# Optimization experiments

Hardware: AMD Instinct MI355X
Metric: run time of the kernel (lower is better)

## Reference

```python
import jax, jax.numpy as jnp
import numpy as np

B, C, L = 256, 512, 150
CI = C // 4            # channel_in = in_dim // 4 = 128
K = 150                # one_hot_cls_num (depthwise kernel over length)
POOL = 150             # MaxPool2d kernel (150, 1)
EPS = 1e-5             # BatchNorm eps


def setup_inputs() -> dict:
    key = jax.random.key(0)
    ks = jax.random.split(key, 8)
    n = lambda k, shape, s: jax.random.normal(k, shape, jnp.float32) * s
    return {
        "x":    jax.random.normal(ks[0], (B, C, L, 1), jnp.float32),
        "Wv":   n(ks[1], (CI, C), 0.06),   "bv": jnp.zeros((CI,), jnp.float32),
        "Wq":   n(ks[2], (CI, CI), 0.12),  "bq": jnp.zeros((CI,), jnp.float32),
        "Wk":   n(ks[3], (CI, CI), 0.12),  "bk": jnp.zeros((CI,), jnp.float32),
        "gamma": n(ks[4], (), 1.0),
        "Wd":   n(ks[5], (2 * CI, K), 0.1), "bd": jnp.zeros((2 * CI,), jnp.float32),
        "Wp":   n(ks[6], (2 * CI, 2 * CI), 0.08), "bp": jnp.zeros((2 * CI,), jnp.float32),
        "bn_g": jnp.ones((2 * CI,), jnp.float32),
        "bn_b": jnp.zeros((2 * CI,), jnp.float32),
    }


def reference(x, Wv, bv, Wq, bq, Wk, bk, gamma, Wd, bd, Wp, bp, bn_g, bn_b):
    xb = x[..., 0]                                             # [B, C, L] (trailing width==1)
    # 1x1 convs are per-position matmuls over the channel dim
    v = jnp.einsum('oc,bcl->bol', Wv, xb) + bv[:, None]        # [B, CI, L]
    q = jnp.einsum('oc,bcl->bol', Wq, v) + bq[:, None]         # [B, CI, L]
    k = jnp.einsum('oc,bcl->bol', Wk, v) + bk[:, None]         # [B, CI, L]
    # raw (unscaled) attention: energy = q^T k, softmax over keys
    energy = jnp.einsum('bci,bcj->bij', q, k)                  # [B, L, L]
    attn = jax.nn.softmax(energy, axis=-1)
    # x = bmm(v, attn^T): out[b,c,i] = sum_j v[b,c,j] * attn[b,i,j]
    att_out = jnp.einsum('bcj,bij->bci', v, attn)              # [B, CI, L]
    cat = jnp.concatenate([gamma * att_out, v], axis=1)        # [B, 2CI, L]
    # MaxPool2d kernel=(150,1), stride=(150,1) over length
    Lp = L // POOL
    y = cat[:, :, : Lp * POOL].reshape(B, 2 * CI, Lp, POOL).max(axis=-1)
    y = y.reshape(B, -1)                                       # [B, 2CI*Lp]
    # depthwise conv kernel (K,1), VALID padding, groups = 2CI
    dw = jax.lax.conv_general_dilated(
        cat[:, :, :, None],                                    # [B, 2CI, L, 1]
        Wd[:, None, :, None],                                  # [2CI, 1, K, 1]
        window_strides=(1, 1), padding='VALID',
        dimension_numbers=('NCHW', 'OIHW', 'NCHW'),
        feature_group_count=2 * CI,
    ) + bd[None, :, None, None]                                # [B, 2CI, L-K+1, 1]
    # pointwise 1x1 conv
    pw = jnp.einsum('oc,bchw->bohw', Wp, dw) + bp[None, :, None, None]
    # BatchNorm2d in training mode: per-channel batch stats (biased variance)
    mean = pw.mean(axis=(0, 2, 3))
    var = pw.var(axis=(0, 2, 3))
    xn = (pw - mean[None, :, None, None]) * jax.lax.rsqrt(var[None, :, None, None] + EPS)
    out = jax.nn.relu(xn * bn_g[None, :, None, None] + bn_b[None, :, None, None])
    return jnp.concatenate([out.reshape(B, -1), y], axis=1)    # [B, 2CI*(L-K+1) + 2CI*Lp]
```

## Files before the change

### kernel.cpp

```cpp
#include <hip/hip_runtime.h>


typedef float f32x4  __attribute__((ext_vector_type(4)));
typedef float f32x16 __attribute__((ext_vector_type(16)));
typedef short s16x8  __attribute__((ext_vector_type(8)));
typedef unsigned short BF;

union U8 { s16x8 v; BF u[8]; uint2 d[2]; unsigned w[4]; };

__device__ __forceinline__ BF bfhi(float f) { return (BF)(__float_as_uint(f) >> 16); }
__device__ __forceinline__ float bff(BF h) { return __uint_as_float(((unsigned)h) << 16); }
__device__ __forceinline__ BF bflo(float f, BF hi) { return bfhi(f - bff(hi)); }
__device__ __forceinline__ BF bfrne(float f) {
    unsigned u = __float_as_uint(f);
    u += 0x7fffu + ((u >> 16) & 1u);
    return (BF)(u >> 16);
}
__device__ __forceinline__ s16x8 ld8l(const BF* p) {
    U8 t; t.d[0] = *(const uint2*)p; t.d[1] = *(const uint2*)(p + 4); return t.v;
}
__device__ __forceinline__ void st4(BF* p, BF a, BF b, BF c, BF d) {
    uint2 t; t.x = (unsigned)a | ((unsigned)b << 16);
    t.y = (unsigned)c | ((unsigned)d << 16);
    *(uint2*)p = t;
}
__device__ __forceinline__ void ldv8(const unsigned* p, s16x8& hi, s16x8& lo) {
    unsigned u[8];
    *(uint4*)&u[0] = *(const uint4*)p;
    *(uint4*)&u[4] = *(const uint4*)(p + 4);
    U8 H, L;
    #pragma unroll
    for (int e = 0; e < 4; ++e) {
        unsigned a = u[2*e], b2 = u[2*e + 1];
        H.w[e] = (a >> 16) | (b2 & 0xffff0000u);
        L.w[e] = (a & 0xffffu) | (b2 << 16);
    }
    hi = H.v; lo = L.v;
}
__device__ __forceinline__ unsigned packf(float f) {
    BF h = bfhi(f);
    return ((unsigned)h << 16) | (unsigned)bflo(f, h);
}
#define MFMA(a, b, c)   __builtin_amdgcn_mfma_f32_16x16x32_bf16(a, b, c, 0, 0, 0)
#define MFMA32(a, b, c) __builtin_amdgcn_mfma_f32_32x32x16_bf16(a, b, c, 0, 0, 0)

__global__ __launch_bounds__(256)
void prep_all(const float* __restrict__ Wv, const float* __restrict__ Wq,
              const float* __restrict__ Wk, const float* __restrict__ bq,
              BF* __restrict__ wvh, BF* __restrict__ wvl,
              BF* __restrict__ wqh, BF* __restrict__ wql,
              float* __restrict__ cvec)
{
    __shared__ float qs[128][33], ks_[128][33];
    const int blk = blockIdx.x, tid = threadIdx.x;
    if (blk < 64) {
        int i = blk * 1024 + tid * 4;
        float4 v = *(const float4*)(Wv + i);
        BF h0 = bfhi(v.x), h1 = bfhi(v.y), h2 = bfhi(v.z), h3 = bfhi(v.w);
        st4(&wvh[i], h0, h1, h2, h3);
        st4(&wvl[i], bflo(v.x,h0), bflo(v.y,h1), bflo(v.z,h2), bflo(v.w,h3));
    } else if (blk < 80) {
        int bi = blk - 64;
        int d1_0 = (bi >> 2) * 32, d2_0 = (bi & 3) * 32;
        for (int i = tid; i < 4096; i += 256) {
            int o = i >> 5, c = i & 31;
            qs[o][c]  = Wq[o * 128 + d1_0 + c];
            ks_[o][c] = Wk[o * 128 + d2_0 + c];
        }
        __syncthreads();
        #pragma unroll
        for (int j = 0; j < 4; ++j) {
            int idx = j * 256 + tid;
            int d1 = idx >> 5, d2 = idx & 31;
            float s = 0.f;
            #pragma unroll 8
            for (int o = 0; o < 128; ++o) s = fmaf(qs[o][d1], ks_[o][d2], s);
            BF h = bfhi(s);
            wqh[(d1_0 + d1) * 128 + d2_0 + d2] = h;
            wql[(d1_0 + d1) * 128 + d2_0 + d2] = bflo(s, h);
        }
    } else {
        if (tid < 128) {
            float s = 0.f;
            for (int o = 0; o < 128; ++o) s += bq[o] * Wk[o * 128 + tid];
            cvec[tid] = s;
        }
    }
}

__global__ __launch_bounds__(1024, 4)
void fused_attn(const float* __restrict__ x, const BF* __restrict__ wvh,
                const BF* __restrict__ wvl, const float* __restrict__ bv,
                const BF* __restrict__ wqh, const BF* __restrict__ wql,
                const float* __restrict__ cvec, const float* __restrict__ gammap,
                const float* __restrict__ Wd, float* __restrict__ dw,
                float* __restrict__ out)
{
    __shared__ char smem[161792];
    BF (*vh)[140] = (BF(*)[140])smem;
    BF (*vl)[140] = (BF(*)[140])(smem + 44800);
    BF (*xt)[2][160][40] = (BF(*)[2][160][40])(smem + 89600);
    unsigned (*ts32)[192][44] = (unsigned(*)[192][44])(smem + 89600);
    BF (*P)[168] = (BF(*)[168])(smem + 44800);
    float* mg   = (float*)(smem + 157184);
    float* sg   = (float*)(smem + 159104);
    float* svec = (float*)(smem + 161024);

    const int b = blockIdx.x;
    const float* xb = x + (long)b * 76800;
    const int tid = threadIdx.x;
    const int lane = tid & 63, w = tid >> 6;
    const int li = lane & 15, gq = lane >> 4;
    const float gamma = gammap[0];

    if (w < 8) {
        const int wm = w & 1, wn = w >> 1;
        f32x4 acc[5][2];
        #pragma unroll
        for (int mf = 0; mf < 5; ++mf)
            #pragma unroll
            for (int nf = 0; nf < 2; ++nf) acc[mf][nf] = f32x4{0.f,0.f,0.f,0.f};
        s16x8 bh[2], bl[2];
        #pragma unroll
        for (int nf = 0; nf < 2; ++nf) {
            long g = (long)(wn*32 + nf*16 + li)*512 + gq*8;
            bh[nf] = *(const s16x8*)(wvh + g);
            bl[nf] = *(const s16x8*)(wvl + g);
        }
        __syncthreads();
        for (int p = 0; p < 16; ++p) {
            s16x8 nbh[2], nbl[2];
            if (p < 15) {
                #pragma unroll
                for (int nf = 0; nf < 2; ++nf) {
                    long g = (long)(wn*32 + nf*16 + li)*512 + (p+1)*32 + gq*8;
                    nbh[nf] = *(const s16x8*)(wvh + g);
                    nbl[nf] = *(const s16x8*)(wvl + g);
                }
            }
            const BF (*xh)[40]  = xt[p & 1][0];
            const BF (*xl2)[40] = xt[p & 1][1];
            __builtin_amdgcn_s_setprio(1);
            #pragma unroll
            for (int mf = 0; mf < 5; ++mf) {
                int row = wm*80 + mf*16 + li;
                s16x8 ah = *(const s16x8*)&xh[row][gq*8];
                s16x8 al = *(const s16x8*)&xl2[row][gq*8];
                #pragma unroll
                for (int nf = 0; nf < 2; ++nf) {
                    acc[mf][nf] = MFMA(al, bh[nf], acc[mf][nf]);
                    acc[mf][nf] = MFMA(ah, bl[nf], acc[mf][nf]);
                    acc[mf][nf] = MFMA(ah, bh[nf], acc[mf][nf]);
                }
            }
            __builtin_amdgcn_s_setprio(0);
            if (p < 15) {
                #pragma unroll
                for (int nf = 0; nf < 2; ++nf) { bh[nf] = nbh[nf]; bl[nf] = nbl[nf]; }
            }
            __syncthreads();
        }
        #pragma unroll
        for (int nf = 0; nf < 2; ++nf) {
            int c = wn*32 + nf*16 + li;
            float bvv = bv[c];
            #pragma unroll
            for (int mf = 0; mf < 5; ++mf)
                #pragma unroll
                for (int r = 0; r < 4; ++r) {
                    int l = wm*80 + mf*16 + gq*4 + r;
                    float f = acc[mf][nf][r] + bvv;
                    BF h = bfhi(f);
                    vh[l][c] = h;
                    vl[l][c] = bflo(f, h);
                }
        }
    } else {
        const int sw = w - 8;
        float cur[3][4];
        auto ldchunk = [&](int p) {
            #pragma unroll
            for (int it = 0; it < 3; ++it) {
                int l = it*64 + lane;
                #pragma unroll
                for (int cc = 0; cc < 4; ++cc)
                    cur[it][cc] = (l < 150) ? xb[(p*32 + sw*4 + cc)*150 + l] : 0.f;
            }
        };
        auto wrchunk = [&](int buf) {
            #pragma unroll
            for (int it = 0; it < 3; ++it) {
                int l = it*64 + lane;
                if (l < 160) {
                    BF h0=bfhi(cur[it][0]), h1=bfhi(cur[it][1]);
                    BF h2=bfhi(cur[it][2]), h3=bfhi(cur[it][3]);
                    st4(&xt[buf][0][l][sw*4], h0, h1, h2, h3);
                    st4(&xt[buf][1][l][sw*4], bflo(cur[it][0],h0), bflo(cur[it][1],h1),
                                              bflo(cur[it][2],h2), bflo(cur[it][3],h3));
                }
            }
        };
        ldchunk(0); wrchunk(0); ldchunk(1);
        __syncthreads();
        for (int p = 0; p < 16; ++p) {
            if (p < 15) {
                wrchunk((p + 1) & 1);
                if (p < 14) ldchunk(p + 2);
            }
            __syncthreads();
        }
    }
    __syncthreads();

    f32x4 eacc[2][4];
    #pragma unroll
    for (int a = 0; a < 2; ++a)
        #pragma unroll
        for (int b2 = 0; b2 < 4; ++b2) eacc[a][b2] = f32x4{0.f,0.f,0.f,0.f};
    const int iw = w / 3, jw = w % 3;
    const int l31 = lane & 31, hi5 = lane >> 5;

    for (int pr = 0; pr < 2; ++pr) {
        if (w < 10) {
            const int s2 = w / 5, jt = w % 5;
            const int ss = pr*2 + s2;
            f32x16 tacc;
            #pragma unroll
            for (int r = 0; r < 16; ++r) tacc[r] = 0.f;
            const int cg2 = ss*32 + l31;
            const int jr0 = jt*32 + l31;
            __builtin_amdgcn_s_setprio(1);
            #pragma unroll
            for (int kc = 0; kc < 8; ++kc) {
                int kof = kc*16 + hi5*8;
                s16x8 bh = *(const s16x8*)(wqh + (long)cg2*128 + kof);
                s16x8 bl = *(const s16x8*)(wql + (long)cg2*128 + kof);
                s16x8 ah = ld8l(&vh[jr0][kof]);
                s16x8 al = ld8l(&vl[jr0][kof]);
                tacc = MFMA32(al, bh, tacc);
                tacc = MFMA32(ah, bl, tacc);
                tacc = MFMA32(ah, bh, tacc);
            }
            __builtin_amdgcn_s_setprio(0);
            #pragma unroll
            for (int r = 0; r < 16; ++r) {
                int j = jt*32 + (r & 3) + 8*(r >> 2) + 4*hi5;
                ts32[s2][j][l31] = packf(tacc[r]);
            }
        } else if (pr == 0) {
            int t2 = tid - 640;
            if (t2 < 160) {
                float s = 0.f;
                #pragma unroll
                for (int k = 0; k < 16; ++k) {
                    U8 t; t.v = ld8l(&vh[t2][k*8]);
                    #pragma unroll
                    for (int e = 0; e < 8; ++e)
                        s = fmaf(bff(t.u[e]), cvec[k*8 + e], s);
                }
                svec[t2] = s;
            }
        }
        __syncthreads();
        if (w < 15) {
            #pragma unroll
            for (int s2 = 0; s2 < 2; ++s2) {
                int scol = (pr*2 + s2)*32 + gq*8;
                s16x8 ah[2], al[2];
                #pragma unroll
                for (int mf2 = 0; mf2 < 2; ++mf2) {
                    int row = iw*32 + mf2*16 + li;
                    ah[mf2] = ld8l(&vh[row][scol]);
                    al[mf2] = ld8l(&vl[row][scol]);
                }
                #pragma unroll
                for (int nf = 0; nf < 4; ++nf) {
                    int jr = jw*64 + nf*16 + li;
                    s16x8 bh, bl;
                    ldv8(&ts32[s2][jr][gq*8], bh, bl);
                    #pragma unroll
                    for (int mf2 = 0; mf2 < 2; ++mf2) {
                        eacc[mf2][nf] = MFMA(ah[mf2], bh, eacc[mf2][nf]);
                        eacc[mf2][nf] = MFMA(ah[mf2], bl, eacc[mf2][nf]);
                        eacc[mf2][nf] = MFMA(al[mf2], bh, eacc[mf2][nf]);
                    }
                }
            }
        }
        __syncthreads();
    }

    if (w < 15) {
        #pragma unroll
        for (int nf = 0; nf < 4; ++nf) {
            int j = jw*64 + nf*16 + li;
            float sv = svec[j];
            #pragma unroll
            for (int mf2 = 0; mf2 < 2; ++mf2)
                #pragma unroll
                for (int r = 0; r < 4; ++r)
                    eacc[mf2][nf][r] += sv;
        }
        #pragma unroll
        for (int mf2 = 0; mf2 < 2; ++mf2)
            #pragma unroll
            for (int r = 0; r < 4; ++r) {
                int i = iw*32 + mf2*16 + gq*4 + r;
                float m = -3.4e38f;
                #pragma unroll
                for (int nf = 0; nf < 4; ++nf) {
                    int j = jw*64 + nf*16 + li;
                    if (j < 150) m = fmaxf(m, eacc[mf2][nf][r]);
                }
                #pragma unroll
                for (int o = 1; o < 16; o <<= 1) m = fmaxf(m, __shfl_xor(m, o));
                float rs_ = 0.f;
                #pragma unroll
                for (int nf = 0; nf < 4; ++nf) {
                    int j = jw*64 + nf*16 + li;
                    float e = (j < 150) ? __expf(eacc[mf2][nf][r] - m) : 0.f;
                    eacc[mf2][nf][r] = e;
                    rs_ += e;
                }
                #pragma unroll
                for (int o = 1; o < 16; o <<= 1) rs_ += __shfl_xor(rs_, o);
                if (li == 0) { mg[jw*160 + i] = m; sg[jw*160 + i] = rs_; }
            }
    }
    __syncthreads();
    if (w < 15) {
        #pragma unroll
        for (int mf2 = 0; mf2 < 2; ++mf2)
            #pragma unroll
            for (int r = 0; r < 4; ++r) {
                int i = iw*32 + mf2*16 + gq*4 + r;
                float m0 = mg[i], m1 = mg[160 + i], m2 = mg[320 + i];
                float M = fmaxf(fmaxf(m0, m1), m2);
                float S = fmaf(sg[i], __expf(m0 - M),
                          fmaf(sg[160 + i], __expf(m1 - M),
                               sg[320 + i] * __expf(m2 - M)));
                float scale = __expf(mg[jw*160 + i] - M) / S;
                #pragma unroll
                for (int nf = 0; nf < 4; ++nf) {
                    int j = jw*64 + nf*16 + li;
                    if (j < 160) P[i][j] = bfrne(eacc[mf2][nf][r] * scale);
                }
            }
    }
    __syncthreads();

    {
        const int pc = w & 7, pi = w >> 3;
        f32x4 oacc[5];
        #pragma unroll
        for (int i = 0; i < 5; ++i) oacc[i] = f32x4{0.f,0.f,0.f,0.f};
        #pragma unroll
        for (int ks = 0; ks < 5; ++ks) {
            int c = pc*16 + li;
            int j0 = ks*32 + gq*8;
            U8 t;
            #pragma unroll
            for (int e = 0; e < 8; ++e) t.u[e] = vh[j0 + e][c];
            #pragma unroll
            for (int nf2 = 0; nf2 < 5; ++nf2) {
                int ir = pi*80 + nf2*16 + li;
                s16x8 bp = ld8l(&P[ir][ks*32 + gq*8]);
                oacc[nf2] = MFMA(t.v, bp, oacc[nf2]);
            }
        }

        float* pmax = mg;
        float* pdot = sg;
        #pragma unroll
        for (int r = 0; r < 4; ++r) {
            int c = pc*16 + gq*4 + r;
            float mx = -3.4e38f, dt = 0.f;
            #pragma unroll
            for (int nf2 = 0; nf2 < 5; ++nf2) {
                int l = pi*80 + nf2*16 + li;
                if (l < 150) {
                    float val = gamma * oacc[nf2][r];
                    mx = fmaxf(mx, val);
                    dt = fmaf(val, Wd[c*150 + l], dt);
                }
            }
            #pragma unroll
            for (int o = 1; o < 16; o <<= 1) {
                mx = fmaxf(mx, __shfl_xor(mx, o));
                dt += __shfl_xor(dt, o);
            }
            if (li == 0) { pmax[pi*128 + c] = mx; pdot[pi*128 + c] = dt; }
        }
        __syncthreads();
        if (tid < 128) {
            out[(long)b*512 + 256 + tid] = fmaxf(pmax[tid], pmax[128 + tid]);
            dw[b*256 + tid] = pdot[tid] + pdot[128 + tid];
        } else if (tid >= 256 && tid < 768) {
            int t2 = tid - 256, c2 = t2 >> 2, q3 = t2 & 3;
            int l0 = (q3*150) >> 2, l1 = ((q3 + 1)*150) >> 2;
            float mx = -3.4e38f, dt = 0.f;
            for (int l = l0; l < l1; ++l) {
                float val = bff(vh[l][c2]);
                mx = fmaxf(mx, val);
                dt = fmaf(val, Wd[(128 + c2)*150 + l], dt);
            }
            mx = fmaxf(mx, __shfl_xor(mx, 1));
            dt += __shfl_xor(dt, 1);
            mx = fmaxf(mx, __shfl_xor(mx, 2));
            dt += __shfl_xor(dt, 2);
            if (q3 == 0) {
                out[(long)b*512 + 256 + 128 + c2] = mx;
                dw[b*256 + 128 + c2] = dt;
            }
        }
    }
}

__global__ __launch_bounds__(256)
void tail_pwbn(const float* __restrict__ dw, const float* __restrict__ Wp,
               const float* __restrict__ bn_g, const float* __restrict__ bn_b,
               float* __restrict__ out)
{
    __shared__ float wp_s[256];
    __shared__ float rs[4], rs2[4];
    const int o = blockIdx.x, t = threadIdx.x;
    const int lane = t & 63, w = t >> 6;
    wp_s[t] = Wp[o * 256 + t];
    __syncthreads();
    const float4* dr = (const float4*)(dw + (long)t * 256);
    float acc = 0.f;
    #pragma unroll 8
    for (int i = 0; i < 64; ++i) {
        float4 d4 = dr[i];
        acc = fmaf(d4.x, wp_s[i*4+0], acc);
        acc = fmaf(d4.y, wp_s[i*4+1], acc);
        acc = fmaf(d4.z, wp_s[i*4+2], acc);
        acc = fmaf(d4.w, wp_s[i*4+3], acc);
    }
    float s = acc, s2 = acc * acc;
    #pragma unroll
    for (int d = 1; d < 64; d <<= 1) { s += __shfl_xor(s, d); s2 += __shfl_xor(s2, d); }
    if (lane == 0) { rs[w] = s; rs2[w] = s2; }
    __syncthreads();
    float S  = rs[0] + rs[1] + rs[2] + rs[3];
    float S2 = rs2[0] + rs2[1] + rs2[2] + rs2[3];
    float mean = S * (1.f/256.f);
    float var  = S2 * (1.f/256.f) - mean * mean;
    float sc = rsqrtf(var + 1e-5f) * bn_g[o];
    float sh = bn_b[o] - mean * sc;
    out[(long)t * 512 + o] = fmaxf(fmaf(acc, sc, sh), 0.f);
}

extern "C" void kernel_launch(void* const* d_in, const int* in_sizes, int n_in,
                              void* d_out, int out_size, void* d_ws, size_t ws_size,
                              hipStream_t stream)
{
    (void)in_sizes; (void)n_in; (void)out_size; (void)ws_size;
    const float* x    = (const float*)d_in[0];
    const float* Wv   = (const float*)d_in[1];
    const float* bv   = (const float*)d_in[2];
    const float* Wq   = (const float*)d_in[3];
    const float* bq   = (const float*)d_in[4];
    const float* Wk   = (const float*)d_in[5];
    const float* bk   = (const float*)d_in[6];  (void)bk;
    const float* gam  = (const float*)d_in[7];
    const float* Wd   = (const float*)d_in[8];
    const float* Wp   = (const float*)d_in[10];
    const float* bn_g = (const float*)d_in[12];
    const float* bn_b = (const float*)d_in[13];
    float* out = (float*)d_out;

    char* wsb = (char*)d_ws;
    BF* wvh  = (BF*)wsb;
    BF* wvl  = (BF*)(wsb + 131072);
    BF* wqh  = (BF*)(wsb + 262144);
    BF* wql  = (BF*)(wsb + 294912);
    float* cvec = (float*)(wsb + 327680);
    float* dw   = (float*)(wsb + 328192);

    prep_all<<<81, 256, 0, stream>>>(Wv, Wq, Wk, bq, wvh, wvl, wqh, wql, cvec);
    fused_attn<<<256, 1024, 0, stream>>>(x, wvh, wvl, bv, wqh, wql, cvec,
                                         gam, Wd, dw, out);
    tail_pwbn<<<256, 256, 0, stream>>>(dw, Wp, bn_g, bn_b, out);
}
```

Measured before the change: 88.85 us.

## Fold Wqk into Wv so the energy operand comes straight from x

Precomputes Wt = (Wq^T Wk) · Wv and its bias term in a new prep kernel. The fused kernel can then compute both v and t = Wt·x in the same x-streaming GEMM loop, instead of running a separate per-pair t = Wqk·v MFMA stage that needed a two-pass loop with extra barriers. The energy GEMM now reads t from a packed shared buffer in one pass, and shared-memory layouts were repacked to fit. The trade-off is twice the MFMA work in the first GEMM (K=512 instead of 128 for t), one extra small launch, and different rounding from the reassociated product.

After: 146.0 us. +64.3%, slower.

```diff
diff --git a/kernel.cpp b/kernel.cpp
--- a/kernel.cpp
+++ b/kernel.cpp
@@ -2,7 +2,6 @@
 
 
 typedef float f32x4  __attribute__((ext_vector_type(4)));
-typedef float f32x16 __attribute__((ext_vector_type(16)));
 typedef short s16x8  __attribute__((ext_vector_type(8)));
 typedef unsigned short BF;
 
@@ -41,15 +40,13 @@
     BF h = bfhi(f);
     return ((unsigned)h << 16) | (unsigned)bflo(f, h);
 }
-#define MFMA(a, b, c)   __builtin_amdgcn_mfma_f32_16x16x32_bf16(a, b, c, 0, 0, 0)
-#define MFMA32(a, b, c) __builtin_amdgcn_mfma_f32_32x32x16_bf16(a, b, c, 0, 0, 0)
+#define MFMA(a, b, c) __builtin_amdgcn_mfma_f32_16x16x32_bf16(a, b, c, 0, 0, 0)
 
 __global__ __launch_bounds__(256)
 void prep_all(const float* __restrict__ Wv, const float* __restrict__ Wq,
               const float* __restrict__ Wk, const float* __restrict__ bq,
               BF* __restrict__ wvh, BF* __restrict__ wvl,
-              BF* __restrict__ wqh, BF* __restrict__ wql,
-              float* __restrict__ cvec)
+              float* __restrict__ wqkf, float* __restrict__ cvec)
 {
     __shared__ float qs[128][33], ks_[128][33];
     const int blk = blockIdx.x, tid = threadIdx.x;
@@ -75,9 +72,7 @@
             float s = 0.f;
             #pragma unroll 8
             for (int o = 0; o < 128; ++o) s = fmaf(qs[o][d1], ks_[o][d2], s);
-            BF h = bfhi(s);
-            wqh[(d1_0 + d1) * 128 + d2_0 + d2] = h;
-            wql[(d1_0 + d1) * 128 + d2_0 + d2] = bflo(s, h);
+            wqkf[(d1_0 + d1) * 128 + d2_0 + d2] = s;
         }
     } else {
         if (tid < 128) {
@@ -88,23 +83,59 @@
     }
 }
 
+__global__ __launch_bounds__(256)
+void prep2(const float* __restrict__ wqkf, const float* __restrict__ Wv,
+           const float* __restrict__ bv,
+           BF* __restrict__ wth, BF* __restrict__ wtl, float* __restrict__ tb)
+{
+    __shared__ float a[32][129];
+    __shared__ float bsh[128][132];
+    const int blk = blockIdx.x, tid = threadIdx.x;
+    if (blk < 16) {
+        const int c0 = (blk >> 2) * 32, C0 = (blk & 3) * 128;
+        for (int i = tid; i < 4096; i += 256)
+            a[i >> 7][i & 127] = wqkf[(c0 + (i >> 7)) * 128 + (i & 127)];
+        for (int i = tid; i < 16384; i += 256)
+            bsh[i >> 7][i & 127] = Wv[(i >> 7) * 512 + C0 + (i & 127)];
+        __syncthreads();
+        #pragma unroll
+        for (int o = 0; o < 16; ++o) {
+            int idx = o * 256 + tid;
+            int cp = idx >> 7, Cc = idx & 127;
+            float s = 0.f;
+            #pragma unroll 8
+            for (int d = 0; d < 128; ++d) s = fmaf(a[cp][d], bsh[d][Cc], s);
+            BF h = bfhi(s);
+            long go = (long)(c0 + cp) * 512 + C0 + Cc;
+            wth[go] = h;
+            wtl[go] = bflo(s, h);
+        }
+    } else {
+        if (tid < 128) {
+            float s = 0.f;
+            for (int d = 0; d < 128; ++d) s += wqkf[tid * 128 + d] * bv[d];
+            tb[tid] = s;
+        }
+    }
+}
+
 __global__ __launch_bounds__(1024, 4)
 void fused_attn(const float* __restrict__ x, const BF* __restrict__ wvh,
-                const BF* __restrict__ wvl, const float* __restrict__ bv,
-                const BF* __restrict__ wqh, const BF* __restrict__ wql,
-                const float* __restrict__ cvec, const float* __restrict__ gammap,
-                const float* __restrict__ Wd, float* __restrict__ dw,
-                float* __restrict__ out)
+                const BF* __restrict__ wvl, const BF* __restrict__ wth,
+                const BF* __restrict__ wtl, const float* __restrict__ bv,
+                const float* __restrict__ tb, const float* __restrict__ cvec,
+                const float* __restrict__ gammap, const float* __restrict__ Wd,
+                float* __restrict__ dw, float* __restrict__ out)
 {
-    __shared__ char smem[161792];
-    BF (*vh)[140] = (BF(*)[140])smem;
-    BF (*vl)[140] = (BF(*)[140])(smem + 44800);
-    BF (*xt)[2][160][40] = (BF(*)[2][160][40])(smem + 89600);
-    unsigned (*ts32)[192][44] = (unsigned(*)[192][44])(smem + 89600);
-    BF (*P)[168] = (BF(*)[168])(smem + 44800);
-    float* mg   = (float*)(smem + 157184);
-    float* sg   = (float*)(smem + 159104);
-    float* svec = (float*)(smem + 161024);
+    __shared__ char smem[160224];
+    BF (*vh)[132] = (BF(*)[132])smem;
+    BF (*vl)[132] = (BF(*)[132])(smem + 40128);
+    unsigned (*tpk)[132] = (unsigned(*)[132])(smem + 80256);
+    BF (*xt)[2][160][36] = (BF(*)[2][160][36])(smem + 80256);
+    BF (*P)[168] = (BF(*)[168])(smem + 40128);
+    float* mg   = (float*)(smem + 112000);
+    float* sg   = (float*)(smem + 114048);
+    float* svec = (float*)(smem + 159456);
 
     const int b = blockIdx.x;
     const float* xb = x + (long)b * 76800;
@@ -114,94 +145,78 @@
     const float gamma = gammap[0];
 
     if (w < 8) {
-        const int wm = w & 1, wn = w >> 1;
-        f32x4 acc[5][2];
-        #pragma unroll
-        for (int mf = 0; mf < 5; ++mf)
-            #pragma unroll
-            for (int nf = 0; nf < 2; ++nf) acc[mf][nf] = f32x4{0.f,0.f,0.f,0.f};
-        s16x8 bh[2], bl[2];
-        #pragma unroll
-        for (int nf = 0; nf < 2; ++nf) {
-            long g = (long)(wn*32 + nf*16 + li)*512 + gq*8;
-            bh[nf] = *(const s16x8*)(wvh + g);
-            bl[nf] = *(const s16x8*)(wvl + g);
-        }
+        const int c = w * 16 + li;
+        f32x4 av[10], at[10];
+        #pragma unroll
+        for (int mf = 0; mf < 10; ++mf) { av[mf] = f32x4{0.f,0.f,0.f,0.f}; at[mf] = f32x4{0.f,0.f,0.f,0.f}; }
         __syncthreads();
+        #pragma unroll
         for (int p = 0; p < 16; ++p) {
-            s16x8 nbh[2], nbl[2];
-            if (p < 15) {
-                #pragma unroll
-                for (int nf = 0; nf < 2; ++nf) {
-                    long g = (long)(wn*32 + nf*16 + li)*512 + (p+1)*32 + gq*8;
-                    nbh[nf] = *(const s16x8*)(wvh + g);
-                    nbl[nf] = *(const s16x8*)(wvl + g);
-                }
-            }
-            const BF (*xh)[40]  = xt[p & 1][0];
-            const BF (*xl2)[40] = xt[p & 1][1];
+            long g = (long)c * 512 + p * 32 + gq * 8;
+            s16x8 bh = *(const s16x8*)(wvh + g);
+            s16x8 bl = *(const s16x8*)(wvl + g);
+            s16x8 th = *(const s16x8*)(wth + g);
+            s16x8 tl = *(const s16x8*)(wtl + g);
+            const BF (*xh)[36]  = xt[p & 1][0];
+            const BF (*xl2)[36] = xt[p & 1][1];
             __builtin_amdgcn_s_setprio(1);
             #pragma unroll
-            for (int mf = 0; mf < 5; ++mf) {
-                int row = wm*80 + mf*16 + li;
-                s16x8 ah = *(const s16x8*)&xh[row][gq*8];
-                s16x8 al = *(const s16x8*)&xl2[row][gq*8];
-                #pragma unroll
-                for (int nf = 0; nf < 2; ++nf) {
-                    acc[mf][nf] = MFMA(al, bh[nf], acc[mf][nf]);
-                    acc[mf][nf] = MFMA(ah, bl[nf], acc[mf][nf]);
-                    acc[mf][nf] = MFMA(ah, bh[nf], acc[mf][nf]);
-                }
+            for (int mf = 0; mf < 10; ++mf) {
+                int row = mf * 16 + li;
+                s16x8 ah = ld8l(&xh[row][gq * 8]);
+                s16x8 al = ld8l(&xl2[row][gq * 8]);
+                av[mf] = MFMA(al, bh, av[mf]);
+                av[mf] = MFMA(ah, bl, av[mf]);
+                av[mf] = MFMA(ah, bh, av[mf]);
+                at[mf] = MFMA(al, th, at[mf]);
+                at[mf] = MFMA(ah, tl, at[mf]);
+                at[mf] = MFMA(ah, th, at[mf]);
             }
             __builtin_amdgcn_s_setprio(0);
-            if (p < 15) {
-                #pragma unroll
-                for (int nf = 0; nf < 2; ++nf) { bh[nf] = nbh[nf]; bl[nf] = nbl[nf]; }
-            }
             __syncthreads();
         }
-        #pragma unroll
-        for (int nf = 0; nf < 2; ++nf) {
-            int c = wn*32 + nf*16 + li;
-            float bvv = bv[c];
-            #pragma unroll
-            for (int mf = 0; mf < 5; ++mf)
-                #pragma unroll
-                for (int r = 0; r < 4; ++r) {
-                    int l = wm*80 + mf*16 + gq*4 + r;
-                    float f = acc[mf][nf][r] + bvv;
-                    BF h = bfhi(f);
+        float bvv = bv[c], tbv = tb[c];
+        #pragma unroll
+        for (int mf = 0; mf < 10; ++mf)
+            #pragma unroll
+            for (int r = 0; r < 4; ++r) {
+                int l = mf * 16 + gq * 4 + r;
+                float fv = av[mf][r] + bvv;
+                if (l < 152) {
+                    BF h = bfhi(fv);
                     vh[l][c] = h;
-                    vl[l][c] = bflo(f, h);
-                }
-        }
+                    vl[l][c] = bflo(fv, h);
+                }
+                if (l < 150) tpk[l][c] = packf(at[mf][r] + tbv);
+            }
     } else {
         const int sw = w - 8;
         float cur[3][4];
         auto ldchunk = [&](int p) {
             #pragma unroll
             for (int it = 0; it < 3; ++it) {
-                int l = it*64 + lane;
+                int l = it * 64 + lane;
                 #pragma unroll
                 for (int cc = 0; cc < 4; ++cc)
-                    cur[it][cc] = (l < 150) ? xb[(p*32 + sw*4 + cc)*150 + l] : 0.f;
+                    cur[it][cc] = (l < 150) ? xb[(p * 32 + sw * 4 + cc) * 150 + l] : 0.f;
             }
         };
         auto wrchunk = [&](int buf) {
             #pragma unroll
             for (int it = 0; it < 3; ++it) {
-                int l = it*64 + lane;
+                int l = it * 64 + lane;
                 if (l < 160) {
-                    BF h0=bfhi(cur[it][0]), h1=bfhi(cur[it][1]);
-                    BF h2=bfhi(cur[it][2]), h3=bfhi(cur[it][3]);
-                    st4(&xt[buf][0][l][sw*4], h0, h1, h2, h3);
-                    st4(&xt[buf][1][l][sw*4], bflo(cur[it][0],h0), bflo(cur[it][1],h1),
-                                              bflo(cur[it][2],h2), bflo(cur[it][3],h3));
+                    BF h0 = bfhi(cur[it][0]), h1 = bfhi(cur[it][1]);
+                    BF h2 = bfhi(cur[it][2]), h3 = bfhi(cur[it][3]);
+                    st4(&xt[buf][0][l][sw * 4], h0, h1, h2, h3);
+                    st4(&xt[buf][1][l][sw * 4], bflo(cur[it][0],h0), bflo(cur[it][1],h1),
+                                                bflo(cur[it][2],h2), bflo(cur[it][3],h3));
                 }
             }
         };
         ldchunk(0); wrchunk(0); ldchunk(1);
         __syncthreads();
+        #pragma unroll
         for (int p = 0; p < 16; ++p) {
             if (p < 15) {
                 wrchunk((p + 1) & 1);
@@ -218,82 +233,57 @@
         #pragma unroll
         for (int b2 = 0; b2 < 4; ++b2) eacc[a][b2] = f32x4{0.f,0.f,0.f,0.f};
     const int iw = w / 3, jw = w % 3;
-    const int l31 = lane & 31, hi5 = lane >> 5;
-
-    for (int pr = 0; pr < 2; ++pr) {
-        if (w < 10) {
-            const int s2 = w / 5, jt = w % 5;
-            const int ss = pr*2 + s2;
-            f32x16 tacc;
-            #pragma unroll
-            for (int r = 0; r < 16; ++r) tacc[r] = 0.f;
-            const int cg2 = ss*32 + l31;
-            const int jr0 = jt*32 + l31;
-            __builtin_amdgcn_s_setprio(1);
-            #pragma unroll
-            for (int kc = 0; kc < 8; ++kc) {
-                int kof = kc*16 + hi5*8;
-                s16x8 bh = *(const s16x8*)(wqh + (long)cg2*128 + kof);
-                s16x8 bl = *(const s16x8*)(wql + (long)cg2*128 + kof);
-                s16x8 ah = ld8l(&vh[jr0][kof]);
-                s16x8 al = ld8l(&vl[jr0][kof]);
-                tacc = MFMA32(al, bh, tacc);
-                tacc = MFMA32(ah, bl, tacc);
-                tacc = MFMA32(ah, bh, tacc);
-            }
-            __builtin_amdgcn_s_setprio(0);
-            #pragma unroll
-            for (int r = 0; r < 16; ++r) {
-                int j = jt*32 + (r & 3) + 8*(r >> 2) + 4*hi5;
-                ts32[s2][j][l31] = packf(tacc[r]);
-            }
-        } else if (pr == 0) {
-            int t2 = tid - 640;
-            if (t2 < 160) {
+
+    if (w < 15) {
+        #pragma unroll
+        for (int s = 0; s < 4; ++s) {
+            int scol = s * 32 + gq * 8;
+            s16x8 ah[2], al[2];
+            #pragma unroll
+            for (int mf2 = 0; mf2 < 2; ++mf2) {
+                int row = iw * 32 + mf2 * 16 + li;
+                row = (row < 152) ? row : 151;
+                ah[mf2] = ld8l(&vh[row][scol]);
+                al[mf2] = ld8l(&vl[row][scol]);
+            }
+            #pragma unroll
+            for (int nf = 0; nf < 4; ++nf) {
+                int jr = jw * 64 + nf * 16 + li;
+                jr = (jr < 150) ? jr : 149;
+                s16x8 bh, bl;
+                ldv8(&tpk[jr][scol], bh, bl);
+                #pragma unroll
+                for (int mf2 = 0; mf2 < 2; ++mf2) {
+                    eacc[mf2][nf] = MFMA(ah[mf2], bh, eacc[mf2][nf]);
+                    eacc[mf2][nf] = MFMA(ah[mf2], bl, eacc[mf2][nf]);
+                    eacc[mf2][nf] = MFMA(al[mf2], bh, eacc[mf2][nf]);
+                }
+            }
+        }
+    } else {
+        #pragma unroll
+        for (int rep = 0; rep < 3; ++rep) {
+            int j = lane + rep * 64;
+            if (j < 152) {
                 float s = 0.f;
                 #pragma unroll
                 for (int k = 0; k < 16; ++k) {
-                    U8 t; t.v = ld8l(&vh[t2][k*8]);
+                    U8 t; t.v = ld8l(&vh[j][k * 8]);
                     #pragma unroll
                     for (int e = 0; e < 8; ++e)
-                        s = fmaf(bff(t.u[e]), cvec[k*8 + e], s);
-                }
-                svec[t2] = s;
-            }
-        }
-        __syncthreads();
-        if (w < 15) {
-            #pragma unroll
-            for (int s2 = 0; s2 < 2; ++s2) {
-                int scol = (pr*2 + s2)*32 + gq*8;
-                s16x8 ah[2], al[2];
-                #pragma unroll
-                for (int mf2 = 0; mf2 < 2; ++mf2) {
-                    int row = iw*32 + mf2*16 + li;
-                    ah[mf2] = ld8l(&vh[row][scol]);
-                    al[mf2] = ld8l(&vl[row][scol]);
-                }
-                #pragma unroll
-                for (int nf = 0; nf < 4; ++nf) {
-                    int jr = jw*64 + nf*16 + li;
-                    s16x8 bh, bl;
-                    ldv8(&ts32[s2][jr][gq*8], bh, bl);
-                    #pragma unroll
-                    for (int mf2 = 0; mf2 < 2; ++mf2) {
-                        eacc[mf2][nf] = MFMA(ah[mf2], bh, eacc[mf2][nf]);
-                        eacc[mf2][nf] = MFMA(ah[mf2], bl, eacc[mf2][nf]);
-                        eacc[mf2][nf] = MFMA(al[mf2], bh, eacc[mf2][nf]);
-                    }
-                }
-            }
-        }
-        __syncthreads();
-    }
+                        s = fmaf(bff(t.u[e]), cvec[k * 8 + e], s);
+                }
+                svec[j] = s;
+            }
+        }
+        if (lane < 40) svec[152 + lane] = 0.f;
+    }
+    __syncthreads();
 
     if (w < 15) {
         #pragma unroll
         for (int nf = 0; nf < 4; ++nf) {
-            int j = jw*64 + nf*16 + li;
+            int j = jw * 64 + nf * 16 + li;
             float sv = svec[j];
             #pragma unroll
             for (int mf2 = 0; mf2 < 2; ++mf2)
@@ -305,11 +295,11 @@
         for (int mf2 = 0; mf2 < 2; ++mf2)
             #pragma unroll
             for (int r = 0; r < 4; ++r) {
-                int i = iw*32 + mf2*16 + gq*4 + r;
+                int i = iw * 32 + mf2 * 16 + gq * 4 + r;
                 float m = -3.4e38f;
                 #pragma unroll
                 for (int nf = 0; nf < 4; ++nf) {
-                    int j = jw*64 + nf*16 + li;
+                    int j = jw * 64 + nf * 16 + li;
                     if (j < 150) m = fmaxf(m, eacc[mf2][nf][r]);
                 }
                 #pragma unroll
@@ -317,14 +307,14 @@
                 float rs_ = 0.f;
                 #pragma unroll
                 for (int nf = 0; nf < 4; ++nf) {
-                    int j = jw*64 + nf*16 + li;
+                    int j = jw * 64 + nf * 16 + li;
                     float e = (j < 150) ? __expf(eacc[mf2][nf][r] - m) : 0.f;
                     eacc[mf2][nf][r] = e;
                     rs_ += e;
                 }
                 #pragma unroll
                 for (int o = 1; o < 16; o <<= 1) rs_ += __shfl_xor(rs_, o);
-                if (li == 0) { mg[jw*160 + i] = m; sg[jw*160 + i] = rs_; }
+                if (li == 0) { mg[jw * 160 + i] = m; sg[jw * 160 + i] = rs_; }
             }
     }
     __syncthreads();
@@ -333,16 +323,16 @@
         for (int mf2 = 0; mf2 < 2; ++mf2)
             #pragma unroll
             for (int r = 0; r < 4; ++r) {
-                int i = iw*32 + mf2*16 + gq*4 + r;
+                int i = iw * 32 + mf2 * 16 + gq * 4 + r;
                 float m0 = mg[i], m1 = mg[160 + i], m2 = mg[320 + i];
                 float M = fmaxf(fmaxf(m0, m1), m2);
                 float S = fmaf(sg[i], __expf(m0 - M),
                           fmaf(sg[160 + i], __expf(m1 - M),
                                sg[320 + i] * __expf(m2 - M)));
-                float scale = __expf(mg[jw*160 + i] - M) / S;
+                float scale = __expf(mg[jw * 160 + i] - M) / S;
                 #pragma unroll
                 for (int nf = 0; nf < 4; ++nf) {
-                    int j = jw*64 + nf*16 + li;
+                    int j = jw * 64 + nf * 16 + li;
                     if (j < 160) P[i][j] = bfrne(eacc[mf2][nf][r] * scale);
                 }
             }
@@ -356,15 +346,19 @@
         for (int i = 0; i < 5; ++i) oacc[i] = f32x4{0.f,0.f,0.f,0.f};
         #pragma unroll
         for (int ks = 0; ks < 5; ++ks) {
-            int c = pc*16 + li;
-            int j0 = ks*32 + gq*8;
+            int c = pc * 16 + li;
+            int j0 = ks * 32 + gq * 8;
             U8 t;
             #pragma unroll
-            for (int e = 0; e < 8; ++e) t.u[e] = vh[j0 + e][c];
+            for (int e = 0; e < 8; ++e) {
+                int jj = j0 + e;
+                jj = (jj < 152) ? jj : 151;
+                t.u[e] = vh[jj][c];
+            }
             #pragma unroll
             for (int nf2 = 0; nf2 < 5; ++nf2) {
-                int ir = pi*80 + nf2*16 + li;
-                s16x8 bp = ld8l(&P[ir][ks*32 + gq*8]);
+                int ir = pi * 80 + nf2 * 16 + li;
+                s16x8 bp = ld8l(&P[ir][ks * 32 + gq * 8]);
                 oacc[nf2] = MFMA(t.v, bp, oacc[nf2]);
             }
         }
@@ -373,15 +367,15 @@
         float* pdot = sg;
         #pragma unroll
         for (int r = 0; r < 4; ++r) {
-            int c = pc*16 + gq*4 + r;
+            int c = pc * 16 + gq * 4 + r;
             float mx = -3.4e38f, dt = 0.f;
             #pragma unroll
             for (int nf2 = 0; nf2 < 5; ++nf2) {
-                int l = pi*80 + nf2*16 + li;
+                int l = pi * 80 + nf2 * 16 + li;
                 if (l < 150) {
                     float val = gamma * oacc[nf2][r];
                     mx = fmaxf(mx, val);
-                    dt = fmaf(val, Wd[c*150 + l], dt);
+                    dt = fmaf(val, Wd[c * 150 + l], dt);
                 }
             }
             #pragma unroll
@@ -389,28 +383,28 @@
                 mx = fmaxf(mx, __shfl_xor(mx, o));
                 dt += __shfl_xor(dt, o);
             }
-            if (li == 0) { pmax[pi*128 + c] = mx; pdot[pi*128 + c] = dt; }
+            if (li == 0) { pmax[pi * 128 + c] = mx; pdot[pi * 128 + c] = dt; }
         }
         __syncthreads();
         if (tid < 128) {
-            out[(long)b*512 + 256 + tid] = fmaxf(pmax[tid], pmax[128 + tid]);
-            dw[b*256 + tid] = pdot[tid] + pdot[128 + tid];
+            out[(long)b * 512 + 256 + tid] = fmaxf(pmax[tid], pmax[128 + tid]);
+            dw[b * 256 + tid] = pdot[tid] + pdot[128 + tid];
         } else if (tid >= 256 && tid < 768) {
             int t2 = tid - 256, c2 = t2 >> 2, q3 = t2 & 3;
-            int l0 = (q3*150) >> 2, l1 = ((q3 + 1)*150) >> 2;
+            int l0 = (q3 * 150) >> 2, l1 = ((q3 + 1) * 150) >> 2;
             float mx = -3.4e38f, dt = 0.f;
             for (int l = l0; l < l1; ++l) {
                 float val = bff(vh[l][c2]);
                 mx = fmaxf(mx, val);
-                dt = fmaf(val, Wd[(128 + c2)*150 + l], dt);
+                dt = fmaf(val, Wd[(128 + c2) * 150 + l], dt);
             }
             mx = fmaxf(mx, __shfl_xor(mx, 1));
             dt += __shfl_xor(dt, 1);
             mx = fmaxf(mx, __shfl_xor(mx, 2));
             dt += __shfl_xor(dt, 2);
             if (q3 == 0) {
-                out[(long)b*512 + 256 + 128 + c2] = mx;
-                dw[b*256 + 128 + c2] = dt;
+                out[(long)b * 512 + 256 + 128 + c2] = mx;
+                dw[b * 256 + 128 + c2] = dt;
             }
         }
     }
@@ -471,15 +465,18 @@
     float* out = (float*)d_out;
 
     char* wsb = (char*)d_ws;
-    BF* wvh  = (BF*)wsb;
-    BF* wvl  = (BF*)(wsb + 131072);
-    BF* wqh  = (BF*)(wsb + 262144);
-    BF* wql  = (BF*)(wsb + 294912);
-    float* cvec = (float*)(wsb + 327680);
-    float* dw   = (float*)(wsb + 328192);
-
-    prep_all<<<81, 256, 0, stream>>>(Wv, Wq, Wk, bq, wvh, wvl, wqh, wql, cvec);
-    fused_attn<<<256, 1024, 0, stream>>>(x, wvh, wvl, bv, wqh, wql, cvec,
+    BF* wvh   = (BF*)wsb;
+    BF* wvl   = (BF*)(wsb + 131072);
+    BF* wth   = (BF*)(wsb + 262144);
+    BF* wtl   = (BF*)(wsb + 393216);
+    float* wqkf = (float*)(wsb + 524288);
+    float* cvec = (float*)(wsb + 589824);
+    float* tb   = (float*)(wsb + 590336);
+    float* dw   = (float*)(wsb + 590848);
+
+    prep_all<<<81, 256, 0, stream>>>(Wv, Wq, Wk, bq, wvh, wvl, wqkf, cvec);
+    prep2<<<17, 256, 0, stream>>>(wqkf, Wv, bv, wth, wtl, tb);
+    fused_attn<<<256, 1024, 0, stream>>>(x, wvh, wvl, wth, wtl, bv, tb, cvec,
                                          gam, Wd, dw, out);
     tail_pwbn<<<256, 256, 0, stream>>>(dw, Wp, bn_g, bn_b, out);
 }
```
